# Performance work log

Measured on AMD Instinct MI355X. Metric: run time of the kernel, lower is better.

## Reference

```python
import jax, jax.numpy as jnp
import numpy as np

B, H, W, DIM = 8, 128, 128, 96
MED = 2 * DIM            # med_channels
NS = 3                   # num_scales
SCTX = 48                # spatial context channels
RIN = DIM + SCTX         # reweight mlp input
RHID = int(0.25 * RIN)   # 36
ROUT = NS * MED          # 576
FH, FWH = H, W // 2 + 1  # rfft2 output grid
SCALE_HW = [(16, 9), (8, 4), (24, 13)]  # per-scale filter resolutions


def _cubic(t, a=-0.75):
    t = abs(t)
    if t <= 1.0:
        return (a + 2) * t ** 3 - (a + 3) * t ** 2 + 1.0
    if t < 2.0:
        return a * t ** 3 - 5 * a * t ** 2 + 8 * a * t - 4 * a
    return 0.0


def _resize_mat(old, new):
    # bicubic, align_corners=True, border replication (matches F.interpolate)
    M = np.zeros((new, old), dtype=np.float32)
    for j in range(new):
        s = j * (old - 1) / (new - 1) if new > 1 else 0.0
        f = int(np.floor(s))
        for k in range(-1, 3):
            M[j, min(max(f + k, 0), old - 1)] += _cubic(s - (f + k))
    return jnp.asarray(M)


def _soa(x, scale, bias):
    r = jnp.maximum(x, 0.0)
    return scale * r * r + bias


def setup_inputs() -> dict:
    key = jax.random.key(0)
    ks = jax.random.split(key, 10)
    inp = {
        "x": jax.random.normal(ks[0], (B, H, W, DIM), dtype=jnp.float32),
        "w1": jax.random.normal(ks[1], (MED, DIM), dtype=jnp.float32) * 0.02,
        "soa1_scale": jnp.ones((1,), jnp.float32),
        "soa1_bias": jnp.zeros((1,), jnp.float32),
        "cw0": jax.random.normal(ks[2], (SCALE_HW[0][0], SCALE_HW[0][1], MED, 2), dtype=jnp.float32) * 0.02,
        "cw1": jax.random.normal(ks[3], (SCALE_HW[1][0], SCALE_HW[1][1], MED, 2), dtype=jnp.float32) * 0.02,
        "cw2": jax.random.normal(ks[4], (SCALE_HW[2][0], SCALE_HW[2][1], MED, 2), dtype=jnp.float32) * 0.02,
        "sp_w": jax.random.normal(ks[5], (SCTX, DIM), dtype=jnp.float32) * 0.05,
        "bn_gamma": jnp.ones((SCTX,), jnp.float32),
        "bn_beta": jnp.zeros((SCTX,), jnp.float32),
        "bn_mean": jnp.zeros((SCTX,), jnp.float32),
        "bn_var": jnp.ones((SCTX,), jnp.float32),
        "fc1": jax.random.normal(ks[6], (RHID, RIN), dtype=jnp.float32) * 0.05,
        "mlp_scale": jnp.ones((1,), jnp.float32),
        "mlp_bias": jnp.zeros((1,), jnp.float32),
        "fc2": jax.random.normal(ks[7], (ROUT, RHID), dtype=jnp.float32) * 0.05,
        "w2": jax.random.normal(ks[8], (DIM, MED), dtype=jnp.float32) * 0.02,
    }
    return inp


def reference(x, w1, soa1_scale, soa1_bias, cw0, cw1, cw2, sp_w,
              bn_gamma, bn_beta, bn_mean, bn_var,
              fc1, mlp_scale, mlp_bias, fc2, w2):
    # pwconv1 + Soa act
    x_pre = _soa(jnp.einsum('bhwc,mc->bhwm', x, w1), soa1_scale, soa1_bias)
    # rfft2 over spatial dims (ortho) -> [B, FH, FWH, MED] complex64
    xf = jnp.fft.rfft2(x_pre.transpose(0, 3, 1, 2), axes=(2, 3), norm='ortho').transpose(0, 2, 3, 1)
    # resize each scale's complex weight to the fft grid (bicubic align_corners=True)
    filts = []
    for cw in (cw0, cw1, cw2):
        Rh = _resize_mat(cw.shape[0], FH)
        Rw = _resize_mat(cw.shape[1], FWH)
        t = jnp.einsum('Hh,hwmc->Hwmc', Rh, cw)
        t = jnp.einsum('Ww,Hwmc->HWmc', Rw, t)
        filts.append(jax.lax.complex(t[..., 0], t[..., 1]))
    filt = jnp.stack(filts)  # [NS, FH, FWH, MED] complex64
    # routing context: global channel mean + 1x1 conv / BN(eval) / relu / GAP
    gctx = x.mean(axis=(1, 2))  # [B, DIM]
    y = jnp.einsum('bhwc,sc->bhws', x, sp_w)
    y = (y - bn_mean) * jax.lax.rsqrt(bn_var + 1e-5) * bn_gamma + bn_beta
    sctx = jnp.maximum(y, 0.0).mean(axis=(1, 2))  # [B, SCTX]
    fused = jnp.concatenate([gctx, sctx], axis=1)  # [B, RIN]
    hmid = _soa(fused @ fc1.T, mlp_scale, mlp_bias)
    r = jax.nn.softmax((hmid @ fc2.T).reshape(-1, NS, MED), axis=1)  # [B, NS, MED]
    # routing-weighted combined filter + spectral multiply
    comb = jnp.einsum('shwm,bsm->bhwm', filt, r.astype(filt.dtype))
    xff = xf * comb
    xsp = jnp.fft.irfft2(xff.transpose(0, 3, 1, 2), s=(H, W), axes=(2, 3), norm='ortho').transpose(0, 2, 3, 1)
    # act2 is Identity; pwconv2
    return jnp.einsum('bhwm,cm->bhwc', xsp, w2)
```

## Files before the change

### kernel.cpp

```cpp
#include <hip/hip_runtime.h>
#include <math.h>

#define BB    8
#define HH    128
#define WW    128
#define DIM   96
#define MED   192
#define HWPX  16384
#define FWH   65
#define LSTR  67

#define P_OFF     0
#define P_SZ      (8*192*16384)
#define FILT_OFF  (P_OFF + P_SZ)
#define FILT_SZ   (3*192*128*65*2)
#define GS_OFF    (FILT_OFF + FILT_SZ)
#define SS_OFF    (GS_OFF + 768)
#define R_OFF     (SS_OFF + 384)
#define W1B_OFF   (R_OFF + 4608)
#define W2B_OFF   (W1B_OFF + 18432)

typedef __attribute__((ext_vector_type(8))) short short8_t;
typedef __attribute__((ext_vector_type(4))) float float4_t;

__device__ __forceinline__ unsigned short bf16_rne(float f){
  unsigned u = __float_as_uint(f);
  unsigned r = (u + 0x7FFFu + ((u>>16)&1u)) >> 16;
  return (unsigned short)r;
}
__device__ __forceinline__ float bf16_to_f(unsigned short h){
  return __uint_as_float(((unsigned)h) << 16);
}

__global__ __launch_bounds__(256) void k_prep(
    const float* __restrict__ w1, const float* __restrict__ w2,
    unsigned short* __restrict__ W1B, unsigned short* __restrict__ W2B)
{
  int tid = threadIdx.x + blockIdx.x*256;
  int nthr = 256*36;
  for (int i = tid; i < 2*3*12*512; i += nthr) {
    int j = i & 7, l = (i>>3) & 63;
    int nt = (i>>9) % 12, kc = ((i>>9)/12) % 3, term = i / (3*12*512);
    int mp = nt*16 + (l&15);
    int c  = kc*32 + (l>>4)*8 + j;
    float v = w1[mp*96 + c];
    unsigned short hi = bf16_rne(v);
    W1B[i] = (term==0) ? hi : bf16_rne(v - bf16_to_f(hi));
  }
  for (int i = tid; i < 2*6*6*512; i += nthr) {
    int j = i & 7, l = (i>>3) & 63;
    int nt = (i>>9) % 6, kc = ((i>>9)/6) % 6, term = i / (6*6*512);
    int cp = nt*16 + (l&15);
    int m  = kc*32 + (l>>4)*8 + j;
    float v = w2[cp*192 + m];
    unsigned short hi = bf16_rne(v);
    W2B[i] = (term==0) ? hi : bf16_rne(v - bf16_to_f(hi));
  }
}

__global__ __launch_bounds__(256) void k_route1(
    const float* __restrict__ x, const float* __restrict__ sp_w,
    const float* __restrict__ bn_gamma, const float* __restrict__ bn_beta,
    const float* __restrict__ bn_mean, const float* __restrict__ bn_var,
    float* __restrict__ gsum, float* __restrict__ ssum)
{
  __shared__ __align__(16) float xt[96*68];
  __shared__ __align__(16) float spwt[96*52];
  __shared__ float sacc[48];
  int t = threadIdx.x;
  int b = blockIdx.x >> 6;
  int chunk = blockIdx.x & 63;
  int p0 = chunk * 256;

  for (int i = t; i < 48*96; i += 256) { int s = i/96, c = i%96; spwt[c*52+s] = sp_w[i]; }
  if (t < 48) sacc[t] = 0.f;

  int sg  = t >> 4;
  int pi4 = (t & 15) * 4;
  float bnA[4], bnB[4];
  if (t < 192) {
    #pragma unroll
    for (int q=0;q<4;q++){
      int s = sg*4+q;
      float a = bn_gamma[s] * rsqrtf(bn_var[s] + 1e-5f);
      bnA[q]=a; bnB[q]=bn_beta[s] - bn_mean[s]*a;
    }
  }
  float greg = 0.f;
  float sreg[4] = {0.f,0.f,0.f,0.f};

  for (int tile = 0; tile < 4; ++tile) {
    __syncthreads();
    const float* src = x + ((size_t)b*HWPX + p0 + tile*64) * 96;
    for (int i = t; i < 64*96/4; i += 256) {
      float4 v = ((const float4*)src)[i];
      int flat = i*4; int p = flat/96, c = flat%96;
      xt[(c+0)*68+p]=v.x; xt[(c+1)*68+p]=v.y; xt[(c+2)*68+p]=v.z; xt[(c+3)*68+p]=v.w;
    }
    __syncthreads();
    if (t < 96) {
      const float4* col = (const float4*)&xt[t*68];
      float s0=0,s1=0,s2=0,s3=0;
      #pragma unroll
      for (int j=0;j<16;j++){ float4 v = col[j]; s0+=v.x; s1+=v.y; s2+=v.z; s3+=v.w; }
      greg += (s0+s1)+(s2+s3);
    }
    if (t < 192) {
      float acc[4][4] = {};
      for (int c = 0; c < 96; ++c) {
        float4 xv = *(const float4*)&xt[c*68 + pi4];
        float4 wv = *(const float4*)&spwt[c*52 + sg*4];
        float xa[4] = {xv.x,xv.y,xv.z,xv.w};
        float wa[4] = {wv.x,wv.y,wv.z,wv.w};
        #pragma unroll
        for (int ii=0;ii<4;ii++)
          #pragma unroll
          for (int jj=0;jj<4;jj++)
            acc[ii][jj] = fmaf(xa[ii], wa[jj], acc[ii][jj]);
      }
      #pragma unroll
      for (int q=0;q<4;q++)
        #pragma unroll
        for (int pp=0;pp<4;pp++) {
          float yb = acc[pp][q]*bnA[q] + bnB[q];
          sreg[q] += fmaxf(yb, 0.f);
        }
    }
  }
  __syncthreads();
  if (t < 192) { for (int q=0;q<4;q++) atomicAdd(&sacc[sg*4+q], sreg[q]); }
  if (t < 96) atomicAdd(&gsum[b*96+t], greg);
  __syncthreads();
  if (t < 48) atomicAdd(&ssum[b*48+t], sacc[t]);
}

__global__ __launch_bounds__(256) void k_pw1(
    const float* __restrict__ x, const unsigned short* __restrict__ W1B,
    const float* __restrict__ soa_scale, const float* __restrict__ soa_bias,
    float* __restrict__ P)
{
  int t = threadIdx.x;
  int lane = t & 63, wv = t >> 6;
  int px0 = blockIdx.x*64 + wv*16;
  int b = px0 >> 14;
  int pxl = px0 & 16383;

  float4_t acc[12];
  #pragma unroll
  for (int nt=0; nt<12; ++nt) acc[nt] = (float4_t){0.f,0.f,0.f,0.f};

  #pragma unroll
  for (int kc=0; kc<3; ++kc) {
    const float* xp = x + (size_t)(px0 + (lane&15))*96 + kc*32 + (lane>>4)*8;
    float4 v0 = *(const float4*)xp;
    float4 v1 = *(const float4*)(xp+4);
    float vv[8] = {v0.x,v0.y,v0.z,v0.w, v1.x,v1.y,v1.z,v1.w};
    short8_t Bh, Bl;
    #pragma unroll
    for (int j=0;j<8;j++){
      unsigned short h = bf16_rne(vv[j]);
      Bh[j] = (short)h;
      Bl[j] = (short)bf16_rne(vv[j] - bf16_to_f(h));
    }
    const short8_t* a_hi = (const short8_t*)(W1B + (size_t)(0*3+kc)*12*512) + lane;
    const short8_t* a_lo = (const short8_t*)(W1B + (size_t)(1*3+kc)*12*512) + lane;
    #pragma unroll
    for (int nt=0; nt<12; ++nt) {
      short8_t Ah = a_hi[nt*64];
      short8_t Al = a_lo[nt*64];
      acc[nt] = __builtin_amdgcn_mfma_f32_16x16x32_bf16(Ah, Bh, acc[nt], 0,0,0);
      acc[nt] = __builtin_amdgcn_mfma_f32_16x16x32_bf16(Ah, Bl, acc[nt], 0,0,0);
      acc[nt] = __builtin_amdgcn_mfma_f32_16x16x32_bf16(Al, Bh, acc[nt], 0,0,0);
    }
  }
  float sc = soa_scale[0], bi = soa_bias[0];
  #pragma unroll
  for (int nt=0; nt<12; ++nt) {
    #pragma unroll
    for (int q=0;q<4;q++){
      float d = acc[nt][q];
      float v = fmaxf(d, 0.f);
      d = sc*v*v + bi;
      int mp = nt*16 + (lane>>4)*4 + q;
      P[(size_t)(b*192 + mp)*HWPX + pxl + (lane&15)] = d;
    }
  }
}

__global__ __launch_bounds__(256) void k_pw2(
    const float* __restrict__ P, const unsigned short* __restrict__ W2B,
    float* __restrict__ out)
{
  int t = threadIdx.x;
  int lane = t & 63, wv = t >> 6;
  int px0 = blockIdx.x*64 + wv*16;
  int b = px0 >> 14;
  int pxl = px0 & 16383;

  float4_t acc[6];
  #pragma unroll
  for (int nt=0; nt<6; ++nt) acc[nt] = (float4_t){0.f,0.f,0.f,0.f};

  #pragma unroll
  for (int kc=0; kc<6; ++kc) {
    const float* ap = P + (size_t)(b*192 + kc*32 + (lane>>4)*8)*HWPX + pxl + (lane&15);
    short8_t Ah, Al;
    #pragma unroll
    for (int j=0;j<8;j++){
      float v = ap[(size_t)j*HWPX];
      unsigned short h = bf16_rne(v);
      Ah[j] = (short)h;
      Al[j] = (short)bf16_rne(v - bf16_to_f(h));
    }
    const short8_t* b_hi = (const short8_t*)(W2B + (size_t)(0*6+kc)*6*512) + lane;
    const short8_t* b_lo = (const short8_t*)(W2B + (size_t)(1*6+kc)*6*512) + lane;
    #pragma unroll
    for (int nt=0; nt<6; ++nt) {
      short8_t Bh = b_hi[nt*64];
      short8_t Bl = b_lo[nt*64];
      acc[nt] = __builtin_amdgcn_mfma_f32_16x16x32_bf16(Ah, Bh, acc[nt], 0,0,0);
      acc[nt] = __builtin_amdgcn_mfma_f32_16x16x32_bf16(Ah, Bl, acc[nt], 0,0,0);
      acc[nt] = __builtin_amdgcn_mfma_f32_16x16x32_bf16(Al, Bh, acc[nt], 0,0,0);
    }
  }
  #pragma unroll
  for (int nt=0; nt<6; ++nt) {
    #pragma unroll
    for (int q=0;q<4;q++){
      int px = px0 + (lane>>4)*4 + q;
      out[(size_t)px*96 + nt*16 + (lane&15)] = acc[nt][q];
    }
  }
}

__global__ __launch_bounds__(256) void k_route2(
    const float* __restrict__ gsum, const float* __restrict__ ssum,
    const float* __restrict__ fc1, const float* __restrict__ fc2,
    const float* __restrict__ mlp_scale, const float* __restrict__ mlp_bias,
    float* __restrict__ r_out)
{
  __shared__ float fused[144], hmid[36], rpre[576];
  int t = threadIdx.x, b = blockIdx.x;
  if (t < 96) fused[t] = gsum[b*96+t] * (1.f/16384.f);
  else if (t < 144) fused[t] = ssum[b*48 + (t-96)] * (1.f/16384.f);
  __syncthreads();
  if (t < 36) {
    float a = 0.f;
    for (int i=0;i<144;i++) a = fmaf(fused[i], fc1[t*144+i], a);
    float rr = fmaxf(a, 0.f);
    hmid[t] = mlp_scale[0]*rr*rr + mlp_bias[0];
  }
  __syncthreads();
  for (int o = t; o < 576; o += 256) {
    float a = 0.f;
    for (int j=0;j<36;j++) a = fmaf(hmid[j], fc2[o*36+j], a);
    rpre[o] = a;
  }
  __syncthreads();
  if (t < 192) {
    float v0 = rpre[t], v1 = rpre[192+t], v2 = rpre[384+t];
    float mx = fmaxf(v0, fmaxf(v1, v2));
    float e0 = expf(v0-mx), e1 = expf(v1-mx), e2 = expf(v2-mx);
    float inv = 1.f/(e0+e1+e2);
    r_out[(b*3+0)*192+t] = e0*inv;
    r_out[(b*3+1)*192+t] = e1*inv;
    r_out[(b*3+2)*192+t] = e2*inv;
  }
}

__device__ __forceinline__ float cubicw(float tt){
  float t = fabsf(tt), t2=t*t, t3=t2*t;
  if (t <= 1.f) return 1.25f*t3 - 2.25f*t2 + 1.f;
  if (t < 2.f)  return -0.75f*t3 + 3.75f*t2 - 6.f*t + 3.f;
  return 0.f;
}

__global__ __launch_bounds__(256) void k_filt(
    const float* __restrict__ cw0, const float* __restrict__ cw1,
    const float* __restrict__ cw2, float* __restrict__ filt)
{
  int bx = blockIdx.x; int s = bx >> 7; int fh = bx & 127;
  const float* cw = (s==0) ? cw0 : ((s==1) ? cw1 : cw2);
  int SH = (s==0) ? 16 : ((s==1) ? 8 : 24);
  int SW = (s==0) ? 9  : ((s==1) ? 4 : 13);
  float sh = fh * (float)(SH-1) / 127.f;
  int fh0 = (int)floorf(sh);
  float wh[4]; int ih[4];
  #pragma unroll
  for (int k=0;k<4;k++){
    int kk = fh0-1+k;
    wh[k] = cubicw(sh - (float)kk);
    ih[k] = min(max(kk,0), SH-1);
  }
  int t = threadIdx.x;
  for (int i = t; i < 192*65; i += 256) {
    int m = i / 65, fw = i % 65;
    float sw = fw * (float)(SW-1) / 64.f;
    int fw0 = (int)floorf(sw);
    float are=0.f, aim=0.f;
    #pragma unroll
    for (int kb=0;kb<4;kb++){
      int jj = fw0-1+kb;
      float wwb = cubicw(sw - (float)jj);
      int iw = min(max(jj,0), SW-1);
      #pragma unroll
      for (int ka=0;ka<4;ka++){
        const float* p = cw + (size_t)((ih[ka]*SW + iw)*192 + m)*2;
        float wgt = wh[ka]*wwb;
        are = fmaf(wgt, p[0], are);
        aim = fmaf(wgt, p[1], aim);
      }
    }
    *(float2*)&filt[ (size_t)(((s*192+m)*128 + fh)*65 + fw) * 2 ] = make_float2(are, aim);
  }
}

__device__ __forceinline__ void dif4(float* SR, float* SI,
    const float* twr, const float* twi,
    int a0, int a1, int a2, int a3, int t1, int t2, int t3)
{
  float x0r=SR[a0], x0i=SI[a0], x1r=SR[a1], x1i=SI[a1];
  float x2r=SR[a2], x2i=SI[a2], x3r=SR[a3], x3i=SI[a3];
  float ur = x0r+x2r, ui = x0i+x2i, d0r = x0r-x2r, d0i = x0i-x2i;
  float sr = x1r+x3r, si = x1i+x3i, d1r = x1r-x3r, d1i = x1i-x3i;
  float w1r = twr[t1], w1i = twi[t1];
  float wr_ = d0r*w1r - d0i*w1i, wi_ = d0r*w1i + d0i*w1r;
  float w2r = twr[t2], w2i = twi[t2];
  float vr = d1r*w2r - d1i*w2i, vi = d1r*w2i + d1i*w2r;
  float t3r = twr[t3], t3i = twi[t3];
  SR[a0] = ur+sr;  SI[a0] = ui+si;
  float mr = ur-sr, mi = ui-si;
  SR[a1] = mr*t3r - mi*t3i; SI[a1] = mr*t3i + mi*t3r;
  SR[a2] = wr_+vr; SI[a2] = wi_+vi;
  float nr = wr_-vr, ni = wi_-vi;
  SR[a3] = nr*t3r - ni*t3i; SI[a3] = nr*t3i + ni*t3r;
}

__device__ __forceinline__ void dit4(float* SR, float* SI,
    const float* twr, const float* twi,
    int a0, int a1, int a2, int a3, int tA, int tB, int tC)
{
  float x0r=SR[a0], x0i=SI[a0], x1r=SR[a1], x1i=SI[a1];
  float x2r=SR[a2], x2i=SI[a2], x3r=SR[a3], x3i=SI[a3];
  float war = twr[tA], wai = twi[tA];
  float x1tr = x1r*war + x1i*wai, x1ti = x1i*war - x1r*wai;
  float x3tr = x3r*war + x3i*wai, x3ti = x3i*war - x3r*wai;
  float ur = x0r+x1tr, ui = x0i+x1ti, vr = x0r-x1tr, vi = x0i-x1ti;
  float sr = x2r+x3tr, si = x2i+x3ti, wr_ = x2r-x3tr, wi_ = x2i-x3ti;
  float wbr = twr[tB], wbi = twi[tB];
  float str = sr*wbr + si*wbi, sti = si*wbr - sr*wbi;
  float wcr = twr[tC], wci = twi[tC];
  float wtr = wr_*wcr + wi_*wci, wti = wi_*wcr - wr_*wci;
  SR[a0] = ur+str; SI[a0] = ui+sti;
  SR[a2] = ur-str; SI[a2] = ui-sti;
  SR[a1] = vr+wtr; SI[a1] = vi+wti;
  SR[a3] = vr-wtr; SI[a3] = vi-wti;
}

__global__ __launch_bounds__(512, 4) void k_spectral(
    float* __restrict__ P, const float* __restrict__ filt, const float* __restrict__ r)
{
  __shared__ float SR[128*LSTR];
  __shared__ float SI[128*LSTR];
  __shared__ float twr[64], twi[64];
  int t = threadIdx.x;
  int bm = blockIdx.x; int b = bm / 192; int m = bm % 192;
  float* plane = P + (size_t)bm * HWPX;

  if (t < 64) {
    float ang = -6.283185307179586477f * (float)t / 128.f;
    twr[t] = cosf(ang); twi[t] = sinf(ang);
  }
  for (int it = 0; it < 8; ++it) {
    int idx = t + 512*it;
    int h = idx >> 5, j = idx & 31;
    float4 v = ((const float4*)plane)[idx];
    int base = h*LSTR + 2*j;
    SR[base]   = v.x; SI[base]   = v.y;
    SR[base+1] = v.z; SI[base+1] = v.w;
  }
  float r0 = r[(b*3+0)*192+m];
  float r1 = r[(b*3+1)*192+m];
  float r2 = r[(b*3+2)*192+m];
  __syncthreads();

  #pragma unroll
  for (int ps = 0; ps < 3; ++ps) {
    const int lh = 5 - 2*ps;
    const int h1 = 1 << lh, h2 = h1 >> 1;
    for (int it = 0; it < 4; ++it) {
      int idx = t + 512*it;
      int row = idx & 127, g = idx >> 7;
      int k = g & (h2-1), blk = g >> (lh-1);
      int base = row*LSTR + blk*(2*h1) + k;
      dif4(SR,SI,twr,twi, base, base+h2, base+h1, base+h1+h2,
           k << (6-lh), (k+h2) << (6-lh), k << (7-lh));
    }
    __syncthreads();
  }

  for (int it = 0; it < 9; ++it) {
    int idx = t + 512*it;
    if (idx < 128*33) {
      int row = idx & 127, k = idx >> 7;
      int base = row*LSTR;
      if (k == 0) {
        float zr = SR[base], zi = SI[base];
        SR[base]    = zr + zi; SI[base]    = 0.f;
        SR[base+64] = zr - zi; SI[base+64] = 0.f;
      } else {
        int a = __brev((unsigned)k) >> 26;
        int bidx = __brev((unsigned)(64-k)) >> 26;
        float ar = SR[base+a], ai = SI[base+a];
        float br = SR[base+bidx], bi = SI[base+bidx];
        float sr_ = 0.5f*(ar+br), si_ = 0.5f*(ai-bi);
        float dr  = 0.5f*(ar-br), di  = 0.5f*(ai+bi);
        float wr = twr[k], wi = twi[k];
        float tr = wr*di + wi*dr;
        float ti = -(wr*dr - wi*di);
        SR[base+a]    = sr_ + tr; SI[base+a]    = si_ + ti;
        SR[base+bidx] = sr_ - tr; SI[base+bidx] = -si_ + ti;
      }
    }
  }
  __syncthreads();

  #pragma unroll
  for (int ps = 0; ps < 3; ++ps) {
    const int lh = 6 - 2*ps;
    const int h1 = 1 << lh, h2 = h1 >> 1;
    for (int it = 0; it < 5; ++it) {
      int idx = t + 512*it;
      if (idx < 65*32) {
        int g = idx / 65, col = idx - g*65;
        int k = g & (h2-1), blk = g >> (lh-1);
        int p = blk*(2*h1) + k;
        dif4(SR,SI,twr,twi, p*LSTR+col, (p+h2)*LSTR+col, (p+h1)*LSTR+col, (p+h1+h2)*LSTR+col,
             k << (6-lh), (k+h2) << (6-lh), k << (7-lh));
      }
    }
    __syncthreads();
  }
  for (int it = 0; it < 9; ++it) {
    int idx = t + 512*it;
    if (idx < 65*64) {
      int j = idx / 65, col = idx - j*65;
      int a0 = (2*j)*LSTR + col, a1 = a0 + LSTR;
      float ur = SR[a0], ui = SI[a0], vr = SR[a1], vi = SI[a1];
      SR[a0]=ur+vr; SI[a0]=ui+vi; SR[a1]=ur-vr; SI[a1]=ui-vi;
    }
  }
  __syncthreads();

  {
    const float2* fb0 = (const float2*)filt + (size_t)(0*192+m)*8320;
    const float2* fb1 = (const float2*)filt + (size_t)(1*192+m)*8320;
    const float2* fb2 = (const float2*)filt + (size_t)(2*192+m)*8320;
    const float inv = 1.f/8192.f;
    for (int it = 0; it < 17; ++it) {
      int idx = t + 512*it;
      if (idx < 8320) {
        int fh = idx / 65, fw = idx - fh*65;
        float2 f0 = fb0[idx], f1 = fb1[idx], f2 = fb2[idx];
        float cr = (r0*f0.x + r1*f1.x + r2*f2.x) * inv;
        float ci = (r0*f0.y + r1*f1.y + r2*f2.y) * inv;
        int sh = __brev((unsigned)fh) >> 25;
        int sw = (fw == 64) ? 64 : (__brev((unsigned)fw) >> 26);
        int a = sh*LSTR + sw;
        float xr = SR[a], xi = SI[a];
        SR[a] = xr*cr - xi*ci;
        SI[a] = xr*ci + xi*cr;
      }
    }
  }
  __syncthreads();

  #pragma unroll
  for (int ps = 0; ps < 3; ++ps) {
    const int la = 2*ps;
    const int h = 1 << la;
    for (int it = 0; it < 5; ++it) {
      int idx = t + 512*it;
      if (idx < 65*32) {
        int g = idx / 65, col = idx - g*65;
        int k = g & (h-1), blk = g >> la;
        int p = blk*(4*h) + k;
        dit4(SR,SI,twr,twi, p*LSTR+col, (p+h)*LSTR+col, (p+2*h)*LSTR+col, (p+3*h)*LSTR+col,
             k << (6-la), k << (5-la), (k+h) << (5-la));
      }
    }
    __syncthreads();
  }
  for (int it = 0; it < 9; ++it) {
    int idx = t + 512*it;
    if (idx < 65*64) {
      int k = idx / 65, col = idx - k*65;
      int a0 = k*LSTR + col, a1 = a0 + 64*LSTR;
      float ur = SR[a0], ui = SI[a0], xr = SR[a1], xi = SI[a1];
      float wr = twr[k], wi = twi[k];
      float xtr = xr*wr + xi*wi, xti = xi*wr - xr*wi;
      SR[a0]=ur+xtr; SI[a0]=ui+xti; SR[a1]=ur-xtr; SI[a1]=ui-xti;
    }
  }
  __syncthreads();

  for (int it = 0; it < 9; ++it) {
    int idx = t + 512*it;
    if (idx < 128*33) {
      int row = idx & 127, k = idx >> 7;
      int base = row*LSTR;
      if (k == 0) {
        float ar = SR[base];
        float cr = SR[base+64];
        SR[base] = 0.5f*(ar+cr); SI[base] = 0.5f*(ar-cr);
      } else {
        int a = __brev((unsigned)k) >> 26;
        int bidx = __brev((unsigned)(64-k)) >> 26;
        float ar = SR[base+a], ai = SI[base+a];
        float br = SR[base+bidx], bi = SI[base+bidx];
        float sr_ = 0.5f*(ar+br), si_ = 0.5f*(ai-bi);
        float dr  = 0.5f*(ar-br), di  = 0.5f*(ai+bi);
        float wr = twr[k], wi = twi[k];
        float tr2 = wi*dr - wr*di;
        float ti2 = wr*dr + wi*di;
        SR[base+a]    = sr_ + tr2; SI[base+a]    = si_ + ti2;
        SR[base+bidx] = sr_ - tr2; SI[base+bidx] = -si_ + ti2;
      }
    }
  }
  __syncthreads();

  #pragma unroll
  for (int ps = 0; ps < 3; ++ps) {
    const int la = 2*ps;
    const int h = 1 << la;
    for (int it = 0; it < 4; ++it) {
      int idx = t + 512*it;
      int row = idx & 127, g = idx >> 7;
      int k = g & (h-1), blk = g >> la;
      int base = row*LSTR + blk*(4*h) + k;
      dit4(SR,SI,twr,twi, base, base+h, base+2*h, base+3*h,
           k << (6-la), k << (5-la), (k+h) << (5-la));
    }
    __syncthreads();
  }

  for (int it = 0; it < 8; ++it) {
    int idx = t + 512*it;
    int h = idx >> 5, j = idx & 31;
    int base = h*LSTR + 2*j;
    float4 v;
    v.x = SR[base];   v.y = SI[base];
    v.z = SR[base+1]; v.w = SI[base+1];
    ((float4*)plane)[idx] = v;
  }
}

extern "C" void kernel_launch(void* const* d_in, const int* in_sizes, int n_in,
                              void* d_out, int out_size, void* d_ws, size_t ws_size,
                              hipStream_t stream) {
  const float* x          = (const float*)d_in[0];
  const float* w1         = (const float*)d_in[1];
  const float* soa1_scale = (const float*)d_in[2];
  const float* soa1_bias  = (const float*)d_in[3];
  const float* cw0        = (const float*)d_in[4];
  const float* cw1        = (const float*)d_in[5];
  const float* cw2        = (const float*)d_in[6];
  const float* sp_w       = (const float*)d_in[7];
  const float* bn_gamma   = (const float*)d_in[8];
  const float* bn_beta    = (const float*)d_in[9];
  const float* bn_mean    = (const float*)d_in[10];
  const float* bn_var     = (const float*)d_in[11];
  const float* fc1        = (const float*)d_in[12];
  const float* mlp_scale  = (const float*)d_in[13];
  const float* mlp_bias   = (const float*)d_in[14];
  const float* fc2        = (const float*)d_in[15];
  const float* w2         = (const float*)d_in[16];
  float* out = (float*)d_out;

  float* ws   = (float*)d_ws;
  float* P    = ws + P_OFF;
  float* filt = ws + FILT_OFF;
  float* gsum = ws + GS_OFF;
  float* ssum = ws + SS_OFF;
  float* rbuf = ws + R_OFF;
  unsigned short* W1B = (unsigned short*)(ws + W1B_OFF);
  unsigned short* W2B = (unsigned short*)(ws + W2B_OFF);

  hipMemsetAsync(gsum, 0, (768+384)*sizeof(float), stream);

  k_prep   <<<36,   256, 0, stream>>>(w1, w2, W1B, W2B);
  k_route1 <<<512,  256, 0, stream>>>(x, sp_w, bn_gamma, bn_beta, bn_mean, bn_var, gsum, ssum);
  k_pw1    <<<2048, 256, 0, stream>>>(x, W1B, soa1_scale, soa1_bias, P);
  k_route2 <<<8,    256, 0, stream>>>(gsum, ssum, fc1, fc2, mlp_scale, mlp_bias, rbuf);
  k_filt   <<<384,  256, 0, stream>>>(cw0, cw1, cw2, filt);
  k_spectral<<<1536,512, 0, stream>>>(P, filt, rbuf);
  k_pw2    <<<2048, 256, 0, stream>>>(P, W2B, out);
}
```

Before: 431.9 us.

## Fuse routing context reduction into pw1 MFMA and interleave spectral LDS as float2

The separate k_route1 pass over x is removed. The sp_w 1x1 conv is appended as three extra MFMA row tiles in k_pw1, and the channel-mean and BN/ReLU sums are reduced with shuffles and atomics there, so x is read once. The spectral kernel switches from split real/imag LDS arrays to interleaved float2. It also remaps thread-to-row indexing in the row FFT stages and reorders blocks so the batch varies fastest. The trade-offs are more accumulator registers and atomics in pw1, a different LDS bank-access pattern, and the sp_w conv now running in split-bf16 precision.

Result: faster. 419.7 us (-2.8%).

```diff
diff --git a/kernel.cpp b/kernel.cpp
--- a/kernel.cpp
+++ b/kernel.cpp
@@ -18,7 +18,7 @@
 #define SS_OFF    (GS_OFF + 768)
 #define R_OFF     (SS_OFF + 384)
 #define W1B_OFF   (R_OFF + 4608)
-#define W2B_OFF   (W1B_OFF + 18432)
+#define W2B_OFF   (W1B_OFF + 23040)
 
 typedef __attribute__((ext_vector_type(8))) short short8_t;
 typedef __attribute__((ext_vector_type(4))) float float4_t;
@@ -33,17 +33,18 @@
 }
 
 __global__ __launch_bounds__(256) void k_prep(
-    const float* __restrict__ w1, const float* __restrict__ w2,
+    const float* __restrict__ w1, const float* __restrict__ sp_w,
+    const float* __restrict__ w2,
     unsigned short* __restrict__ W1B, unsigned short* __restrict__ W2B)
 {
   int tid = threadIdx.x + blockIdx.x*256;
   int nthr = 256*36;
-  for (int i = tid; i < 2*3*12*512; i += nthr) {
+  for (int i = tid; i < 2*3*15*512; i += nthr) {
     int j = i & 7, l = (i>>3) & 63;
-    int nt = (i>>9) % 12, kc = ((i>>9)/12) % 3, term = i / (3*12*512);
-    int mp = nt*16 + (l&15);
-    int c  = kc*32 + (l>>4)*8 + j;
-    float v = w1[mp*96 + c];
+    int nt = (i>>9) % 15, kc = ((i>>9)/15) % 3, term = i / (3*15*512);
+    int r = nt*16 + (l&15);
+    int c = kc*32 + (l>>4)*8 + j;
+    float v = (r < 192) ? w1[r*96 + c] : sp_w[(r-192)*96 + c];
     unsigned short hi = bf16_rne(v);
     W1B[i] = (term==0) ? hi : bf16_rne(v - bf16_to_f(hi));
   }
@@ -58,103 +59,45 @@
   }
 }
 
-__global__ __launch_bounds__(256) void k_route1(
-    const float* __restrict__ x, const float* __restrict__ sp_w,
-    const float* __restrict__ bn_gamma, const float* __restrict__ bn_beta,
-    const float* __restrict__ bn_mean, const float* __restrict__ bn_var,
-    float* __restrict__ gsum, float* __restrict__ ssum)
-{
-  __shared__ __align__(16) float xt[96*68];
-  __shared__ __align__(16) float spwt[96*52];
-  __shared__ float sacc[48];
-  int t = threadIdx.x;
-  int b = blockIdx.x >> 6;
-  int chunk = blockIdx.x & 63;
-  int p0 = chunk * 256;
-
-  for (int i = t; i < 48*96; i += 256) { int s = i/96, c = i%96; spwt[c*52+s] = sp_w[i]; }
-  if (t < 48) sacc[t] = 0.f;
-
-  int sg  = t >> 4;
-  int pi4 = (t & 15) * 4;
-  float bnA[4], bnB[4];
-  if (t < 192) {
-    #pragma unroll
-    for (int q=0;q<4;q++){
-      int s = sg*4+q;
-      float a = bn_gamma[s] * rsqrtf(bn_var[s] + 1e-5f);
-      bnA[q]=a; bnB[q]=bn_beta[s] - bn_mean[s]*a;
-    }
-  }
-  float greg = 0.f;
-  float sreg[4] = {0.f,0.f,0.f,0.f};
-
-  for (int tile = 0; tile < 4; ++tile) {
-    __syncthreads();
-    const float* src = x + ((size_t)b*HWPX + p0 + tile*64) * 96;
-    for (int i = t; i < 64*96/4; i += 256) {
-      float4 v = ((const float4*)src)[i];
-      int flat = i*4; int p = flat/96, c = flat%96;
-      xt[(c+0)*68+p]=v.x; xt[(c+1)*68+p]=v.y; xt[(c+2)*68+p]=v.z; xt[(c+3)*68+p]=v.w;
-    }
-    __syncthreads();
-    if (t < 96) {
-      const float4* col = (const float4*)&xt[t*68];
-      float s0=0,s1=0,s2=0,s3=0;
-      #pragma unroll
-      for (int j=0;j<16;j++){ float4 v = col[j]; s0+=v.x; s1+=v.y; s2+=v.z; s3+=v.w; }
-      greg += (s0+s1)+(s2+s3);
-    }
-    if (t < 192) {
-      float acc[4][4] = {};
-      for (int c = 0; c < 96; ++c) {
-        float4 xv = *(const float4*)&xt[c*68 + pi4];
-        float4 wv = *(const float4*)&spwt[c*52 + sg*4];
-        float xa[4] = {xv.x,xv.y,xv.z,xv.w};
-        float wa[4] = {wv.x,wv.y,wv.z,wv.w};
-        #pragma unroll
-        for (int ii=0;ii<4;ii++)
-          #pragma unroll
-          for (int jj=0;jj<4;jj++)
-            acc[ii][jj] = fmaf(xa[ii], wa[jj], acc[ii][jj]);
-      }
-      #pragma unroll
-      for (int q=0;q<4;q++)
-        #pragma unroll
-        for (int pp=0;pp<4;pp++) {
-          float yb = acc[pp][q]*bnA[q] + bnB[q];
-          sreg[q] += fmaxf(yb, 0.f);
-        }
-    }
-  }
-  __syncthreads();
-  if (t < 192) { for (int q=0;q<4;q++) atomicAdd(&sacc[sg*4+q], sreg[q]); }
-  if (t < 96) atomicAdd(&gsum[b*96+t], greg);
-  __syncthreads();
-  if (t < 48) atomicAdd(&ssum[b*48+t], sacc[t]);
-}
-
 __global__ __launch_bounds__(256) void k_pw1(
     const float* __restrict__ x, const unsigned short* __restrict__ W1B,
     const float* __restrict__ soa_scale, const float* __restrict__ soa_bias,
-    float* __restrict__ P)
-{
+    const float* __restrict__ bn_gamma, const float* __restrict__ bn_beta,
+    const float* __restrict__ bn_mean, const float* __restrict__ bn_var,
+    float* __restrict__ P, float* __restrict__ gsum, float* __restrict__ ssum)
+{
+  __shared__ float red[4][144];
+  __shared__ float bnA_s[48], bnB_s[48];
   int t = threadIdx.x;
   int lane = t & 63, wv = t >> 6;
+  if (t < 48) {
+    float a = bn_gamma[t] * rsqrtf(bn_var[t] + 1e-5f);
+    bnA_s[t] = a; bnB_s[t] = bn_beta[t] - bn_mean[t]*a;
+  }
   int px0 = blockIdx.x*64 + wv*16;
-  int b = px0 >> 14;
+  int b = (blockIdx.x*64) >> 14;
   int pxl = px0 & 16383;
-
-  float4_t acc[12];
-  #pragma unroll
-  for (int nt=0; nt<12; ++nt) acc[nt] = (float4_t){0.f,0.f,0.f,0.f};
+  int g = lane >> 4;
+
+  float4_t acc[15];
+  #pragma unroll
+  for (int nt=0; nt<15; ++nt) acc[nt] = (float4_t){0.f,0.f,0.f,0.f};
 
   #pragma unroll
   for (int kc=0; kc<3; ++kc) {
-    const float* xp = x + (size_t)(px0 + (lane&15))*96 + kc*32 + (lane>>4)*8;
+    const float* xp = x + (size_t)(px0 + (lane&15))*96 + kc*32 + g*8;
     float4 v0 = *(const float4*)xp;
     float4 v1 = *(const float4*)(xp+4);
     float vv[8] = {v0.x,v0.y,v0.z,v0.w, v1.x,v1.y,v1.z,v1.w};
+    #pragma unroll
+    for (int j=0;j<8;j++){
+      float s = vv[j];
+      s += __shfl_xor(s, 1);
+      s += __shfl_xor(s, 2);
+      s += __shfl_xor(s, 4);
+      s += __shfl_xor(s, 8);
+      if ((lane & 15) == 0) red[wv][kc*32 + g*8 + j] = s;
+    }
     short8_t Bh, Bl;
     #pragma unroll
     for (int j=0;j<8;j++){
@@ -162,10 +105,10 @@
       Bh[j] = (short)h;
       Bl[j] = (short)bf16_rne(vv[j] - bf16_to_f(h));
     }
-    const short8_t* a_hi = (const short8_t*)(W1B + (size_t)(0*3+kc)*12*512) + lane;
-    const short8_t* a_lo = (const short8_t*)(W1B + (size_t)(1*3+kc)*12*512) + lane;
-    #pragma unroll
-    for (int nt=0; nt<12; ++nt) {
+    const short8_t* a_hi = (const short8_t*)(W1B + (size_t)(0*3+kc)*15*512) + lane;
+    const short8_t* a_lo = (const short8_t*)(W1B + (size_t)(1*3+kc)*15*512) + lane;
+    #pragma unroll
+    for (int nt=0; nt<15; ++nt) {
       short8_t Ah = a_hi[nt*64];
       short8_t Al = a_lo[nt*64];
       acc[nt] = __builtin_amdgcn_mfma_f32_16x16x32_bf16(Ah, Bh, acc[nt], 0,0,0);
@@ -181,9 +124,29 @@
       float d = acc[nt][q];
       float v = fmaxf(d, 0.f);
       d = sc*v*v + bi;
-      int mp = nt*16 + (lane>>4)*4 + q;
+      int mp = nt*16 + g*4 + q;
       P[(size_t)(b*192 + mp)*HWPX + pxl + (lane&15)] = d;
     }
+  }
+  #pragma unroll
+  for (int tile=0; tile<3; ++tile) {
+    #pragma unroll
+    for (int q=0;q<4;q++){
+      int s = tile*16 + g*4 + q;
+      float y = acc[12+tile][q];
+      float v = fmaxf(bnA_s[s]*y + bnB_s[s], 0.f);
+      v += __shfl_xor(v, 1);
+      v += __shfl_xor(v, 2);
+      v += __shfl_xor(v, 4);
+      v += __shfl_xor(v, 8);
+      if ((lane & 15) == 0) red[wv][96 + s] = v;
+    }
+  }
+  __syncthreads();
+  if (t < 144) {
+    float s = red[0][t] + red[1][t] + red[2][t] + red[3][t];
+    if (t < 96) atomicAdd(&gsum[b*96 + t], s);
+    else        atomicAdd(&ssum[b*48 + (t-96)], s);
   }
 }
 
@@ -315,69 +278,63 @@
   }
 }
 
-__device__ __forceinline__ void dif4(float* SR, float* SI,
-    const float* twr, const float* twi,
+__device__ __forceinline__ float2 c_add(float2 a, float2 b){ return make_float2(a.x+b.x, a.y+b.y); }
+__device__ __forceinline__ float2 c_sub(float2 a, float2 b){ return make_float2(a.x-b.x, a.y-b.y); }
+__device__ __forceinline__ float2 c_mul(float2 a, float2 w){ return make_float2(a.x*w.x - a.y*w.y, a.x*w.y + a.y*w.x); }
+__device__ __forceinline__ float2 c_mulc(float2 a, float2 w){ return make_float2(a.x*w.x + a.y*w.y, a.y*w.x - a.x*w.y); }
+
+__device__ __forceinline__ void dif4(float2* S, const float2* TW,
     int a0, int a1, int a2, int a3, int t1, int t2, int t3)
 {
-  float x0r=SR[a0], x0i=SI[a0], x1r=SR[a1], x1i=SI[a1];
-  float x2r=SR[a2], x2i=SI[a2], x3r=SR[a3], x3i=SI[a3];
-  float ur = x0r+x2r, ui = x0i+x2i, d0r = x0r-x2r, d0i = x0i-x2i;
-  float sr = x1r+x3r, si = x1i+x3i, d1r = x1r-x3r, d1i = x1i-x3i;
-  float w1r = twr[t1], w1i = twi[t1];
-  float wr_ = d0r*w1r - d0i*w1i, wi_ = d0r*w1i + d0i*w1r;
-  float w2r = twr[t2], w2i = twi[t2];
-  float vr = d1r*w2r - d1i*w2i, vi = d1r*w2i + d1i*w2r;
-  float t3r = twr[t3], t3i = twi[t3];
-  SR[a0] = ur+sr;  SI[a0] = ui+si;
-  float mr = ur-sr, mi = ui-si;
-  SR[a1] = mr*t3r - mi*t3i; SI[a1] = mr*t3i + mi*t3r;
-  SR[a2] = wr_+vr; SI[a2] = wi_+vi;
-  float nr = wr_-vr, ni = wi_-vi;
-  SR[a3] = nr*t3r - ni*t3i; SI[a3] = nr*t3i + ni*t3r;
-}
-
-__device__ __forceinline__ void dit4(float* SR, float* SI,
-    const float* twr, const float* twi,
+  float2 x0=S[a0], x1=S[a1], x2=S[a2], x3=S[a3];
+  float2 u = c_add(x0,x2), d0 = c_sub(x0,x2);
+  float2 s = c_add(x1,x3), d1 = c_sub(x1,x3);
+  float2 w = c_mul(d0, TW[t1]);
+  float2 v = c_mul(d1, TW[t2]);
+  float2 t3w = TW[t3];
+  S[a0] = c_add(u,s);
+  S[a1] = c_mul(c_sub(u,s), t3w);
+  S[a2] = c_add(w,v);
+  S[a3] = c_mul(c_sub(w,v), t3w);
+}
+
+__device__ __forceinline__ void dit4(float2* S, const float2* TW,
     int a0, int a1, int a2, int a3, int tA, int tB, int tC)
 {
-  float x0r=SR[a0], x0i=SI[a0], x1r=SR[a1], x1i=SI[a1];
-  float x2r=SR[a2], x2i=SI[a2], x3r=SR[a3], x3i=SI[a3];
-  float war = twr[tA], wai = twi[tA];
-  float x1tr = x1r*war + x1i*wai, x1ti = x1i*war - x1r*wai;
-  float x3tr = x3r*war + x3i*wai, x3ti = x3i*war - x3r*wai;
-  float ur = x0r+x1tr, ui = x0i+x1ti, vr = x0r-x1tr, vi = x0i-x1ti;
-  float sr = x2r+x3tr, si = x2i+x3ti, wr_ = x2r-x3tr, wi_ = x2i-x3ti;
-  float wbr = twr[tB], wbi = twi[tB];
-  float str = sr*wbr + si*wbi, sti = si*wbr - sr*wbi;
-  float wcr = twr[tC], wci = twi[tC];
-  float wtr = wr_*wcr + wi_*wci, wti = wi_*wcr - wr_*wci;
-  SR[a0] = ur+str; SI[a0] = ui+sti;
-  SR[a2] = ur-str; SI[a2] = ui-sti;
-  SR[a1] = vr+wtr; SI[a1] = vi+wti;
-  SR[a3] = vr-wtr; SI[a3] = vi-wti;
+  float2 x0=S[a0], x1=S[a1], x2=S[a2], x3=S[a3];
+  float2 wA = TW[tA];
+  float2 x1t = c_mulc(x1, wA), x3t = c_mulc(x3, wA);
+  float2 u = c_add(x0,x1t), v = c_sub(x0,x1t);
+  float2 s = c_add(x2,x3t), w = c_sub(x2,x3t);
+  float2 st = c_mulc(s, TW[tB]);
+  float2 wt = c_mulc(w, TW[tC]);
+  S[a0] = c_add(u, st);
+  S[a2] = c_sub(u, st);
+  S[a1] = c_add(v, wt);
+  S[a3] = c_sub(v, wt);
 }
 
 __global__ __launch_bounds__(512, 4) void k_spectral(
     float* __restrict__ P, const float* __restrict__ filt, const float* __restrict__ r)
 {
-  __shared__ float SR[128*LSTR];
-  __shared__ float SI[128*LSTR];
-  __shared__ float twr[64], twi[64];
+  __shared__ float2 S[128*LSTR];
+  __shared__ float2 TW[64];
   int t = threadIdx.x;
-  int bm = blockIdx.x; int b = bm / 192; int m = bm % 192;
-  float* plane = P + (size_t)bm * HWPX;
+  int bm = blockIdx.x;
+  int b = bm & 7; int m = bm >> 3;
+  float* plane = P + ((size_t)b*192 + m) * HWPX;
 
   if (t < 64) {
     float ang = -6.283185307179586477f * (float)t / 128.f;
-    twr[t] = cosf(ang); twi[t] = sinf(ang);
+    TW[t] = make_float2(cosf(ang), sinf(ang));
   }
   for (int it = 0; it < 8; ++it) {
     int idx = t + 512*it;
     int h = idx >> 5, j = idx & 31;
     float4 v = ((const float4*)plane)[idx];
     int base = h*LSTR + 2*j;
-    SR[base]   = v.x; SI[base]   = v.y;
-    SR[base+1] = v.z; SI[base+1] = v.w;
+    S[base]   = make_float2(v.x, v.y);
+    S[base+1] = make_float2(v.z, v.w);
   }
   float r0 = r[(b*3+0)*192+m];
   float r1 = r[(b*3+1)*192+m];
@@ -390,10 +347,10 @@
     const int h1 = 1 << lh, h2 = h1 >> 1;
     for (int it = 0; it < 4; ++it) {
       int idx = t + 512*it;
-      int row = idx & 127, g = idx >> 7;
+      int g = idx & 15, row = idx >> 4;
       int k = g & (h2-1), blk = g >> (lh-1);
       int base = row*LSTR + blk*(2*h1) + k;
-      dif4(SR,SI,twr,twi, base, base+h2, base+h1, base+h1+h2,
+      dif4(S,TW, base, base+h2, base+h1, base+h1+h2,
            k << (6-lh), (k+h2) << (6-lh), k << (7-lh));
     }
     __syncthreads();
@@ -405,21 +362,20 @@
       int row = idx & 127, k = idx >> 7;
       int base = row*LSTR;
       if (k == 0) {
-        float zr = SR[base], zi = SI[base];
-        SR[base]    = zr + zi; SI[base]    = 0.f;
-        SR[base+64] = zr - zi; SI[base+64] = 0.f;
+        float2 z = S[base];
+        S[base]    = make_float2(z.x + z.y, 0.f);
+        S[base+64] = make_float2(z.x - z.y, 0.f);
       } else {
         int a = __brev((unsigned)k) >> 26;
         int bidx = __brev((unsigned)(64-k)) >> 26;
-        float ar = SR[base+a], ai = SI[base+a];
-        float br = SR[base+bidx], bi = SI[base+bidx];
-        float sr_ = 0.5f*(ar+br), si_ = 0.5f*(ai-bi);
-        float dr  = 0.5f*(ar-br), di  = 0.5f*(ai+bi);
-        float wr = twr[k], wi = twi[k];
-        float tr = wr*di + wi*dr;
-        float ti = -(wr*dr - wi*di);
-        SR[base+a]    = sr_ + tr; SI[base+a]    = si_ + ti;
-        SR[base+bidx] = sr_ - tr; SI[base+bidx] = -si_ + ti;
+        float2 A = S[base+a], B = S[base+bidx];
+        float sr_ = 0.5f*(A.x+B.x), si_ = 0.5f*(A.y-B.y);
+        float dr  = 0.5f*(A.x-B.x), di  = 0.5f*(A.y+B.y);
+        float2 w = TW[k];
+        float tr = w.x*di + w.y*dr;
+        float ti = -(w.x*dr - w.y*di);
+        S[base+a]    = make_float2(sr_ + tr,  si_ + ti);
+        S[base+bidx] = make_float2(sr_ - tr, -si_ + ti);
       }
     }
   }
@@ -435,7 +391,7 @@
         int g = idx / 65, col = idx - g*65;
         int k = g & (h2-1), blk = g >> (lh-1);
         int p = blk*(2*h1) + k;
-        dif4(SR,SI,twr,twi, p*LSTR+col, (p+h2)*LSTR+col, (p+h1)*LSTR+col, (p+h1+h2)*LSTR+col,
+        dif4(S,TW, p*LSTR+col, (p+h2)*LSTR+col, (p+h1)*LSTR+col, (p+h1+h2)*LSTR+col,
              k << (6-lh), (k+h2) << (6-lh), k << (7-lh));
       }
     }
@@ -446,8 +402,8 @@
     if (idx < 65*64) {
       int j = idx / 65, col = idx - j*65;
       int a0 = (2*j)*LSTR + col, a1 = a0 + LSTR;
-      float ur = SR[a0], ui = SI[a0], vr = SR[a1], vi = SI[a1];
-      SR[a0]=ur+vr; SI[a0]=ui+vi; SR[a1]=ur-vr; SI[a1]=ui-vi;
+      float2 u = S[a0], v = S[a1];
+      S[a0] = c_add(u,v); S[a1] = c_sub(u,v);
     }
   }
   __syncthreads();
@@ -467,9 +423,8 @@
         int sh = __brev((unsigned)fh) >> 25;
         int sw = (fw == 64) ? 64 : (__brev((unsigned)fw) >> 26);
         int a = sh*LSTR + sw;
-        float xr = SR[a], xi = SI[a];
-        SR[a] = xr*cr - xi*ci;
-        SI[a] = xr*ci + xi*cr;
+        float2 X = S[a];
+        S[a] = make_float2(X.x*cr - X.y*ci, X.x*ci + X.y*cr);
       }
     }
   }
@@ -485,7 +440,7 @@
         int g = idx / 65, col = idx - g*65;
         int k = g & (h-1), blk = g >> la;
         int p = blk*(4*h) + k;
-        dit4(SR,SI,twr,twi, p*LSTR+col, (p+h)*LSTR+col, (p+2*h)*LSTR+col, (p+3*h)*LSTR+col,
+        dit4(S,TW, p*LSTR+col, (p+h)*LSTR+col, (p+2*h)*LSTR+col, (p+3*h)*LSTR+col,
              k << (6-la), k << (5-la), (k+h) << (5-la));
       }
     }
@@ -496,10 +451,9 @@
     if (idx < 65*64) {
       int k = idx / 65, col = idx - k*65;
       int a0 = k*LSTR + col, a1 = a0 + 64*LSTR;
-      float ur = SR[a0], ui = SI[a0], xr = SR[a1], xi = SI[a1];
-      float wr = twr[k], wi = twi[k];
-      float xtr = xr*wr + xi*wi, xti = xi*wr - xr*wi;
-      SR[a0]=ur+xtr; SI[a0]=ui+xti; SR[a1]=ur-xtr; SI[a1]=ui-xti;
+      float2 u = S[a0], xv = S[a1];
+      float2 xt = c_mulc(xv, TW[k]);
+      S[a0] = c_add(u,xt); S[a1] = c_sub(u,xt);
     }
   }
   __syncthreads();
@@ -510,21 +464,20 @@
       int row = idx & 127, k = idx >> 7;
       int base = row*LSTR;
       if (k == 0) {
-        float ar = SR[base];
-        float cr = SR[base+64];
-        SR[base] = 0.5f*(ar+cr); SI[base] = 0.5f*(ar-cr);
+        float ar = S[base].x;
+        float cr = S[base+64].x;
+        S[base] = make_float2(0.5f*(ar+cr), 0.5f*(ar-cr));
       } else {
         int a = __brev((unsigned)k) >> 26;
         int bidx = __brev((unsigned)(64-k)) >> 26;
-        float ar = SR[base+a], ai = SI[base+a];
-        float br = SR[base+bidx], bi = SI[base+bidx];
-        float sr_ = 0.5f*(ar+br), si_ = 0.5f*(ai-bi);
-        float dr  = 0.5f*(ar-br), di  = 0.5f*(ai+bi);
-        float wr = twr[k], wi = twi[k];
-        float tr2 = wi*dr - wr*di;
-        float ti2 = wr*dr + wi*di;
-        SR[base+a]    = sr_ + tr2; SI[base+a]    = si_ + ti2;
-        SR[base+bidx] = sr_ - tr2; SI[base+bidx] = -si_ + ti2;
+        float2 A = S[base+a], B = S[base+bidx];
+        float sr_ = 0.5f*(A.x+B.x), si_ = 0.5f*(A.y-B.y);
+        float dr  = 0.5f*(A.x-B.x), di  = 0.5f*(A.y+B.y);
+        float2 w = TW[k];
+        float tr2 = w.y*dr - w.x*di;
+        float ti2 = w.x*dr + w.y*di;
+        S[base+a]    = make_float2(sr_ + tr2,  si_ + ti2);
+        S[base+bidx] = make_float2(sr_ - tr2, -si_ + ti2);
       }
     }
   }
@@ -536,10 +489,10 @@
     const int h = 1 << la;
     for (int it = 0; it < 4; ++it) {
       int idx = t + 512*it;
-      int row = idx & 127, g = idx >> 7;
+      int g = idx & 15, row = idx >> 4;
       int k = g & (h-1), blk = g >> la;
       int base = row*LSTR + blk*(4*h) + k;
-      dit4(SR,SI,twr,twi, base, base+h, base+2*h, base+3*h,
+      dit4(S,TW, base, base+h, base+2*h, base+3*h,
            k << (6-la), k << (5-la), (k+h) << (5-la));
     }
     __syncthreads();
@@ -549,9 +502,8 @@
     int idx = t + 512*it;
     int h = idx >> 5, j = idx & 31;
     int base = h*LSTR + 2*j;
-    float4 v;
-    v.x = SR[base];   v.y = SI[base];
-    v.z = SR[base+1]; v.w = SI[base+1];
+    float2 z0 = S[base], z1 = S[base+1];
+    float4 v; v.x = z0.x; v.y = z0.y; v.z = z1.x; v.w = z1.y;
     ((float4*)plane)[idx] = v;
   }
 }
@@ -589,9 +541,10 @@
 
   hipMemsetAsync(gsum, 0, (768+384)*sizeof(float), stream);
 
-  k_prep   <<<36,   256, 0, stream>>>(w1, w2, W1B, W2B);
-  k_route1 <<<512,  256, 0, stream>>>(x, sp_w, bn_gamma, bn_beta, bn_mean, bn_var, gsum, ssum);
-  k_pw1    <<<2048, 256, 0, stream>>>(x, W1B, soa1_scale, soa1_bias, P);
+  k_prep   <<<36,   256, 0, stream>>>(w1, sp_w, w2, W1B, W2B);
+  k_pw1    <<<2048, 256, 0, stream>>>(x, W1B, soa1_scale, soa1_bias,
+                                      bn_gamma, bn_beta, bn_mean, bn_var,
+                                      P, gsum, ssum);
   k_route2 <<<8,    256, 0, stream>>>(gsum, ssum, fc1, fc2, mlp_scale, mlp_bias, rbuf);
   k_filt   <<<384,  256, 0, stream>>>(cw0, cw1, cw2, filt);
   k_spectral<<<1536,512, 0, stream>>>(P, filt, rbuf);
```
